# Optimization experiments

Measured on AMD Instinct MI355X. Metric: run time of the kernel, lower is better.

## Reference

```python
import jax, jax.numpy as jnp
import numpy as np

N, E, DIN, H, C = 50000, 800000, 256, 128, 8


def setup_inputs() -> dict:
    key = jax.random.key(0)
    k1, k2, k3, k4 = jax.random.split(key, 4)
    x = jax.random.normal(k1, (N, DIN), dtype=jnp.float32)
    edge_index = jax.random.randint(k2, (2, E), 0, N, dtype=jnp.int64)
    W1 = jax.random.normal(k3, (DIN, H), dtype=jnp.float32) * (1.0 / np.sqrt(DIN))
    b1 = jnp.zeros((H,), dtype=jnp.float32)
    W2 = jax.random.normal(k4, (H, C), dtype=jnp.float32) * (1.0 / np.sqrt(H))
    b2 = jnp.zeros((C,), dtype=jnp.float32)
    return {"x": x, "W1": W1, "b1": b1, "W2": W2, "b2": b2, "edge_index": edge_index}


def reference(x, W1, b1, W2, b2, edge_index):
    n = x.shape[0]
    loop = jnp.arange(n, dtype=edge_index.dtype)
    src = jnp.concatenate([edge_index[0], loop])  # messages flow src -> dst
    dst = jnp.concatenate([edge_index[1], loop])
    # symmetric GCN normalization with self-loops (PyG GCNConv default)
    deg = jax.ops.segment_sum(jnp.ones_like(dst, dtype=x.dtype), dst, num_segments=n)
    dinv = jnp.where(deg > 0, deg ** -0.5, 0.0)
    norm = dinv[src] * dinv[dst]  # [E+N]

    def gcn_layer(h, W, b):
        h = h @ W                                   # [N, d_out]
        msg = norm[:, None] * h[src]                # gather: [E+N, d_out]
        agg = jax.ops.segment_sum(msg, dst, num_segments=n)  # scatter-add
        return agg + b

    h = jax.nn.relu(gcn_layer(x, W1, b1))
    # F.dropout(training=False) is identity in eval mode
    out = gcn_layer(h, W2, b2)
    return jax.nn.log_softmax(out, axis=1)
```

## Files before the change

kernel.cpp:

```cpp
#include <hip/hip_runtime.h>
#include <hip/hip_bf16.h>
#include <hip/hip_fp16.h>
#include <stdint.h>

#define DIN 256
#define HD  128
#define CD  8
#define KCH 64
#define SBW 72
#define CSRW 64
#define ECH 4096
#define CAP 64

typedef __attribute__((ext_vector_type(8))) short bf16x8;
typedef __attribute__((ext_vector_type(4))) float f32x4;

__device__ __forceinline__ float bf2f(unsigned short u) {
    union { unsigned int i; float f; } v; v.i = ((unsigned int)u) << 16; return v.f;
}
__device__ __forceinline__ unsigned short f2bf(float f) {
    union { float f; unsigned int i; } v; v.f = f;
    unsigned int r = v.i + 0x7fffu + ((v.i >> 16) & 1u);
    return (unsigned short)(r >> 16);
}
__device__ __forceinline__ int edge_at(const void* ei, int is64, long long idx) {
    return is64 ? (int)((const long long*)ei)[idx] : ((const int*)ei)[idx];
}

__global__ __launch_bounds__(256) void prep_kernel(
    const float* __restrict__ W1, unsigned short* __restrict__ W1T)
{
    int tg = blockIdx.x * 256 + threadIdx.x;
    if (tg < HD * (DIN / 4)) {
        int n  = tg & (HD - 1);
        int k4 = (tg >> 7) * 4;
        unsigned short v[4];
#pragma unroll
        for (int j = 0; j < 4; j++) v[j] = f2bf(W1[(k4 + j) * HD + n]);
        *reinterpret_cast<unsigned long long*>(W1T + (size_t)n * DIN + k4) =
            ((unsigned long long)v[0]) | ((unsigned long long)v[1] << 16) |
            ((unsigned long long)v[2] << 32) | ((unsigned long long)v[3] << 48);
    }
}

__global__ __launch_bounds__(256) void gemm1_scatter_kernel(
    const float* __restrict__ x, const unsigned short* __restrict__ W1T,
    unsigned short* __restrict__ h, int M,
    const void* __restrict__ ei,
    unsigned int* __restrict__ ebuf, unsigned int* __restrict__ G,
    int E, int N, int G1, int NB)
{
    __shared__ unsigned short w1t[HD * SBW];
    if ((int)blockIdx.x >= G1) {
        int* cur = (int*)w1t;
        const int tid = threadIdx.x;
        cur[tid] = 0;
        __syncthreads();
        const int lane = tid & 63;
        int oddw = ((const int*)ei)[2 * lane + 1];
        unsigned long long zb = __ballot(oddw == 0);
        int is64 = (__popcll(zb) >= 56) ? 1 : 0;
        const int c = (int)blockIdx.x - G1;
        const long long e0 = (long long)c * ECH;
#pragma unroll
        for (int k = 0; k < ECH / 256; k++) {
            long long e = e0 + tid + k * 256;
            if (e < E) {
                int s = edge_at(ei, is64, e);
                int d = edge_at(ei, is64, (long long)E + e);
                if ((unsigned)d < (unsigned)N && (unsigned)s < (unsigned)N) {
                    int b = ((unsigned)d) >> 8;
                    int p = atomicAdd(&cur[b], 1);
                    if (p < CAP)
                        ebuf[((size_t)b * NB + c) * CAP + p] =
                            (unsigned int)s | ((unsigned int)d << 16);
                }
            }
        }
        __syncthreads();
        int v = cur[tid]; if (v > CAP) v = CAP;
        G[(size_t)c * 256 + tid] = (unsigned int)v;
        return;
    }
    const int tid  = threadIdx.x;
    const int lane = tid & 63;
    const int wave = tid >> 6;
    const int quad = lane >> 4;
    const int r15  = lane & 15;
    const long long rowBase = (long long)blockIdx.x * 128 + wave * 32;

    f32x4 acc[2][8];
#pragma unroll
    for (int rt = 0; rt < 2; rt++)
#pragma unroll
        for (int ct = 0; ct < 8; ct++)
#pragma unroll
            for (int i = 0; i < 4; i++) acc[rt][ct][i] = 0.0f;

    for (int kh = 0; kh < DIN / KCH; kh++) {
        __syncthreads();
        for (int c = tid; c < HD * (KCH / 8); c += 256) {
            int n   = c >> 3;
            int kk0 = (c & 7) * 8;
            bf16x8 v = *reinterpret_cast<const bf16x8*>(W1T + (size_t)n * DIN + kh * KCH + kk0);
            *reinterpret_cast<bf16x8*>(&w1t[n * SBW + kk0]) = v;
        }
        __syncthreads();

        for (int ki = 0; ki < KCH / 32; ki++) {
            int kk0 = ki * 32 + quad * 8;
            int kg  = kh * KCH + kk0;
            bf16x8 a[2];
#pragma unroll
            for (int rt = 0; rt < 2; rt++) {
                long long row = rowBase + rt * 16 + r15;
                if (row < M) {
                    const float* xp = x + row * DIN + kg;
                    f32x4 f0 = *reinterpret_cast<const f32x4*>(xp);
                    f32x4 f1 = *reinterpret_cast<const f32x4*>(xp + 4);
#pragma unroll
                    for (int j = 0; j < 4; j++) {
                        a[rt][j]     = (short)f2bf(f0[j]);
                        a[rt][j + 4] = (short)f2bf(f1[j]);
                    }
                } else {
#pragma unroll
                    for (int j = 0; j < 8; j++) a[rt][j] = 0;
                }
            }
#pragma unroll
            for (int ct = 0; ct < 8; ct++) {
                bf16x8 b = *reinterpret_cast<const bf16x8*>(&w1t[(ct * 16 + r15) * SBW + kk0]);
                acc[0][ct] = __builtin_amdgcn_mfma_f32_16x16x32_bf16(a[0], b, acc[0][ct], 0, 0, 0);
                acc[1][ct] = __builtin_amdgcn_mfma_f32_16x16x32_bf16(a[1], b, acc[1][ct], 0, 0, 0);
            }
        }
    }
#pragma unroll
    for (int rt = 0; rt < 2; rt++)
#pragma unroll
        for (int ct = 0; ct < 8; ct++)
#pragma unroll
            for (int i = 0; i < 4; i++) {
                long long row = rowBase + rt * 16 + quad * 4 + i;
                if (row < M) h[row * HD + ct * 16 + r15] = f2bf(acc[rt][ct][i]);
            }
}

__global__ __launch_bounds__(256) void csr_build_kernel(
    const unsigned int* __restrict__ ebuf, const unsigned int* __restrict__ G,
    unsigned short* __restrict__ colf, int* __restrict__ count, int N, int NB)
{
    __shared__ int cnt[256];
    __shared__ int gcnt[256];
    const int b = blockIdx.x;
    const int tid = threadIdx.x;
    cnt[tid] = 0;
    gcnt[tid] = (tid < NB) ? (int)G[(size_t)tid * 256 + b] : 0;
    __syncthreads();
    const size_t basee = (size_t)b * NB * CAP;
    const int tot = NB * CAP;
    for (int idx = tid; idx < tot; idx += 256) {
        int c = idx >> 6;
        int i = idx & (CAP - 1);
        if (i < gcnt[c]) {
            unsigned int e = ebuf[basee + idx];
            int d = (int)(e >> 16);
            int slot = atomicAdd(&cnt[d & 255], 1);
            if (slot < CSRW) colf[(d << 6) + slot] = (unsigned short)(e & 0xFFFFu);
        }
    }
    __syncthreads();
    int n = (b << 8) + tid;
    if (n < N) count[n] = cnt[tid];
}

__global__ __launch_bounds__(256) void scale_kernel(
    const unsigned short* __restrict__ h, const int* __restrict__ count,
    unsigned short* __restrict__ h2, int N)
{
    int t = blockIdx.x * 256 + threadIdx.x;
    if (t >= N * (HD / 8)) return;
    int n = t >> 4;
    int deg = count[n]; if (deg > CSRW) deg = CSRW;
    float dn = rsqrtf((float)deg + 1.0f);
    bf16x8 v = *reinterpret_cast<const bf16x8*>(h + (size_t)t * 8);
    bf16x8 o;
#pragma unroll
    for (int j = 0; j < 8; j++) {
        float f = bf2f((unsigned short)v[j]) * dn;
        __half hf = __float2half(f);
        o[j] = *reinterpret_cast<short*>(&hf);
    }
    *reinterpret_cast<bf16x8*>(h2 + (size_t)t * 8) = o;
}

__global__ __launch_bounds__(256) void agg1_fused_kernel(
    const unsigned short* __restrict__ h2, const int* __restrict__ count,
    const unsigned short* __restrict__ colf, const float* __restrict__ b1,
    const float* __restrict__ W2, float* __restrict__ hw2, int N)
{
    const int lane = threadIdx.x & 63;
    const int n = blockIdx.x * 4 + (threadIdx.x >> 6);
    if (n >= N) return;

    float w2a[CD], w2b[CD];
#pragma unroll
    for (int c = 0; c < CD; c++) {
        w2a[c] = W2[(2 * lane)     * CD + c];
        w2b[c] = W2[(2 * lane + 1) * CD + c];
    }

    int deg = count[n]; if (deg > CSRW) deg = CSRW;
    const float dn = rsqrtf((float)deg + 1.0f);

    union UH { unsigned int u; __half2 h; };
    UH p; p.u = *reinterpret_cast<const unsigned int*>(h2 + ((size_t)n << 7) + 2 * lane);
    float2 pf = __half22float2(p.h);
    float acc0 = pf.x, acc1 = pf.y;

    const int base = n << 6;
    int i = 0;
    for (; i + 7 < deg; i += 8) {
        unsigned long long c0 = *reinterpret_cast<const unsigned long long*>(colf + base + i);
        unsigned long long c1 = *reinterpret_cast<const unsigned long long*>(colf + base + i + 4);
        unsigned int s[8];
#pragma unroll
        for (int j = 0; j < 4; j++) {
            s[j]     = (unsigned int)((c0 >> (16 * j)) & 0xFFFFu);
            s[j + 4] = (unsigned int)((c1 >> (16 * j)) & 0xFFFFu);
        }
        UH hv[8];
#pragma unroll
        for (int j = 0; j < 8; j++)
            hv[j].u = *reinterpret_cast<const unsigned int*>(h2 + ((size_t)s[j] << 7) + 2 * lane);
#pragma unroll
        for (int j = 0; j < 8; j++) {
            float2 f = __half22float2(hv[j].h);
            acc0 += f.x;
            acc1 += f.y;
        }
    }
    for (; i < deg; i++) {
        unsigned int s0 = colf[base + i];
        UH a; a.u = *reinterpret_cast<const unsigned int*>(h2 + ((size_t)s0 << 7) + 2 * lane);
        float2 f = __half22float2(a.h);
        acc0 += f.x;
        acc1 += f.y;
    }

    float v0 = dn * acc0 + b1[2 * lane];     v0 = v0 > 0.0f ? v0 : 0.0f;
    float v1 = dn * acc1 + b1[2 * lane + 1]; v1 = v1 > 0.0f ? v1 : 0.0f;

    float part[CD];
#pragma unroll
    for (int c = 0; c < CD; c++) part[c] = v0 * w2a[c] + v1 * w2b[c];

    float t4[4];
    {
        int hi = lane & 1;
#pragma unroll
        for (int k = 0; k < 4; k++) {
            float send = hi ? part[k] : part[4 + k];
            float recv = __shfl_xor(send, 1, 64);
            t4[k] = (hi ? part[4 + k] : part[k]) + recv;
        }
    }
    float t2[2];
    {
        int hi = (lane >> 1) & 1;
#pragma unroll
        for (int k = 0; k < 2; k++) {
            float send = hi ? t4[k] : t4[2 + k];
            float recv = __shfl_xor(send, 2, 64);
            t2[k] = (hi ? t4[2 + k] : t4[k]) + recv;
        }
    }
    float t1;
    {
        int hi = (lane >> 2) & 1;
        float send = hi ? t2[0] : t2[1];
        float recv = __shfl_xor(send, 4, 64);
        t1 = (hi ? t2[1] : t2[0]) + recv;
    }
    t1 += __shfl_xor(t1, 8, 64);
    t1 += __shfl_xor(t1, 16, 64);
    t1 += __shfl_xor(t1, 32, 64);
    int c = ((lane & 1) << 2) | (lane & 2) | ((lane >> 2) & 1);
    if (lane < CD) hw2[(size_t)n * CD + c] = dn * t1;
}

__global__ __launch_bounds__(256) void agg2_kernel(
    const float* __restrict__ hw2, const int* __restrict__ count,
    const unsigned short* __restrict__ colf, const float* __restrict__ b2,
    float* __restrict__ out, int N) {
    int n = blockIdx.x * 256 + threadIdx.x;
    if (n >= N) return;
    int deg = count[n]; if (deg > CSRW) deg = CSRW;
    float dn = rsqrtf((float)deg + 1.0f);
    f32x4 a0 = *reinterpret_cast<const f32x4*>(hw2 + (size_t)n * CD);
    f32x4 a1 = *reinterpret_cast<const f32x4*>(hw2 + (size_t)n * CD + 4);
    const int base = n << 6;
    int i = 0;
    for (; i + 3 < deg; i += 4) {
        unsigned long long cc = *reinterpret_cast<const unsigned long long*>(colf + base + i);
        unsigned int s0 = (unsigned int)(cc & 0xFFFFu);
        unsigned int s1 = (unsigned int)((cc >> 16) & 0xFFFFu);
        unsigned int s2 = (unsigned int)((cc >> 32) & 0xFFFFu);
        unsigned int s3 = (unsigned int)((cc >> 48) & 0xFFFFu);
        f32x4 b0 = *reinterpret_cast<const f32x4*>(hw2 + (size_t)s0 * CD);
        f32x4 b1v = *reinterpret_cast<const f32x4*>(hw2 + (size_t)s0 * CD + 4);
        f32x4 c0 = *reinterpret_cast<const f32x4*>(hw2 + (size_t)s1 * CD);
        f32x4 c1 = *reinterpret_cast<const f32x4*>(hw2 + (size_t)s1 * CD + 4);
        f32x4 d0 = *reinterpret_cast<const f32x4*>(hw2 + (size_t)s2 * CD);
        f32x4 d1 = *reinterpret_cast<const f32x4*>(hw2 + (size_t)s2 * CD + 4);
        f32x4 e0 = *reinterpret_cast<const f32x4*>(hw2 + (size_t)s3 * CD);
        f32x4 e1 = *reinterpret_cast<const f32x4*>(hw2 + (size_t)s3 * CD + 4);
        a0 += (b0 + c0) + (d0 + e0);
        a1 += (b1v + c1) + (d1 + e1);
    }
    for (; i < deg; i++) {
        unsigned int s0 = colf[base + i];
        a0 += *reinterpret_cast<const f32x4*>(hw2 + (size_t)s0 * CD);
        a1 += *reinterpret_cast<const f32x4*>(hw2 + (size_t)s0 * CD + 4);
    }
    float v[CD];
#pragma unroll
    for (int j = 0; j < 4; j++) {
        v[j]     = dn * a0[j] + b2[j];
        v[4 + j] = dn * a1[j] + b2[4 + j];
    }
    float mx = v[0];
#pragma unroll
    for (int j = 1; j < CD; j++) mx = fmaxf(mx, v[j]);
    float s8 = 0.0f;
#pragma unroll
    for (int j = 0; j < CD; j++) s8 += expf(v[j] - mx);
    float lse = mx + logf(s8);
    f32x4 o0, o1;
#pragma unroll
    for (int j = 0; j < 4; j++) {
        o0[j] = v[j] - lse;
        o1[j] = v[4 + j] - lse;
    }
    *reinterpret_cast<f32x4*>(out + (size_t)n * CD)     = o0;
    *reinterpret_cast<f32x4*>(out + (size_t)n * CD + 4) = o1;
}

extern "C" void kernel_launch(void* const* d_in, const int* in_sizes, int n_in,
                              void* d_out, int out_size, void* d_ws, size_t ws_size,
                              hipStream_t stream) {
    const float* x  = (const float*)d_in[0];
    const float* W1 = (const float*)d_in[1];
    const float* b1 = (const float*)d_in[2];
    const float* W2 = (const float*)d_in[3];
    const float* b2 = (const float*)d_in[4];
    const void*  ei = d_in[5];
    const int N = in_sizes[0] / DIN;
    const int E = in_sizes[5] / 2;
    const int G1 = (N + 127) / 128;
    const int NB = (E + ECH - 1) / ECH;
    const int NBK = (N + 255) / 256;

    char* ws = (char*)d_ws;
    size_t off = 0;
    auto alloc = [&](size_t bytes) -> void* {
        void* p = ws + off;
        off = (off + bytes + 255) & ~(size_t)255;
        return p;
    };
    int*   count = (int*)alloc((size_t)N * 4);
    unsigned short* colf = (unsigned short*)alloc((size_t)N * CSRW * 2);
    unsigned short* h  = (unsigned short*)alloc((size_t)N * HD * 2);
    unsigned short* h2 = (unsigned short*)alloc((size_t)N * HD * 2);
    float* hw2 = (float*)alloc((size_t)N * CD * 4);
    unsigned short* W1T = (unsigned short*)alloc((size_t)HD * DIN * 2);
    unsigned int* G    = (unsigned int*)alloc((size_t)NB * 256 * 4);
    unsigned int* ebuf = (unsigned int*)alloc((size_t)NB * 256 * CAP * 4);

    prep_kernel         <<<32, 256, 0, stream>>>(W1, W1T);
    gemm1_scatter_kernel<<<G1 + NB, 256, 0, stream>>>(x, W1T, h, N, ei, ebuf, G, E, N, G1, NB);
    csr_build_kernel    <<<NBK, 256, 0, stream>>>(ebuf, G, colf, count, N, NB);
    scale_kernel        <<<(N * (HD / 8) + 255) / 256, 256, 0, stream>>>(h, count, h2, N);
    agg1_fused_kernel   <<<(N + 3) / 4, 256, 0, stream>>>(h2, count, colf, b1, W2, hw2, N);
    agg2_kernel         <<<(N + 255) / 256, 256, 0, stream>>>(hw2, count, colf, b2,
                                                              (float*)d_out, N);
}
```

Baseline: 196.0 us.

## Fuse degree scaling into CSR build and preload full neighbor list in aggregation

```diff
diff --git a/kernel.cpp b/kernel.cpp
--- a/kernel.cpp
+++ b/kernel.cpp
@@ -14,6 +14,7 @@
 
 typedef __attribute__((ext_vector_type(8))) short bf16x8;
 typedef __attribute__((ext_vector_type(4))) float f32x4;
+typedef __attribute__((ext_vector_type(4))) unsigned int u32x4;
 
 __device__ __forceinline__ float bf2f(unsigned short u) {
     union { unsigned int i; float f; } v; v.i = ((unsigned int)u) << 16; return v.f;
@@ -149,6 +150,7 @@
 
 __global__ __launch_bounds__(256) void csr_build_kernel(
     const unsigned int* __restrict__ ebuf, const unsigned int* __restrict__ G,
+    const unsigned short* __restrict__ h, unsigned short* __restrict__ h2,
     unsigned short* __restrict__ colf, int* __restrict__ count, int N, int NB)
 {
     __shared__ int cnt[256];
@@ -173,26 +175,23 @@
     __syncthreads();
     int n = (b << 8) + tid;
     if (n < N) count[n] = cnt[tid];
-}
-
-__global__ __launch_bounds__(256) void scale_kernel(
-    const unsigned short* __restrict__ h, const int* __restrict__ count,
-    unsigned short* __restrict__ h2, int N)
-{
-    int t = blockIdx.x * 256 + threadIdx.x;
-    if (t >= N * (HD / 8)) return;
-    int n = t >> 4;
-    int deg = count[n]; if (deg > CSRW) deg = CSRW;
-    float dn = rsqrtf((float)deg + 1.0f);
-    bf16x8 v = *reinterpret_cast<const bf16x8*>(h + (size_t)t * 8);
-    bf16x8 o;
-#pragma unroll
-    for (int j = 0; j < 8; j++) {
-        float f = bf2f((unsigned short)v[j]) * dn;
-        __half hf = __float2half(f);
-        o[j] = *reinterpret_cast<short*>(&hf);
-    }
-    *reinterpret_cast<bf16x8*>(h2 + (size_t)t * 8) = o;
+    for (int t = tid; t < 256 * 16; t += 256) {
+        int ln = t >> 4;
+        int gn = (b << 8) + ln;
+        if (gn < N) {
+            int dg = cnt[ln]; if (dg > CSRW) dg = CSRW;
+            float dnn = rsqrtf((float)dg + 1.0f);
+            bf16x8 v = *reinterpret_cast<const bf16x8*>(h + ((size_t)gn << 7) + (t & 15) * 8);
+            bf16x8 o;
+#pragma unroll
+            for (int j = 0; j < 8; j++) {
+                float f = bf2f((unsigned short)v[j]) * dnn;
+                __half hf = __float2half(f);
+                o[j] = *reinterpret_cast<short*>(&hf);
+            }
+            *reinterpret_cast<bf16x8*>(h2 + ((size_t)gn << 7) + (t & 15) * 8) = o;
+        }
+    }
 }
 
 __global__ __launch_bounds__(256) void agg1_fused_kernel(
@@ -204,54 +203,52 @@
     const int n = blockIdx.x * 4 + (threadIdx.x >> 6);
     if (n >= N) return;
 
-    float w2a[CD], w2b[CD];
-#pragma unroll
-    for (int c = 0; c < CD; c++) {
-        w2a[c] = W2[(2 * lane)     * CD + c];
-        w2b[c] = W2[(2 * lane + 1) * CD + c];
-    }
-
     int deg = count[n]; if (deg > CSRW) deg = CSRW;
     const float dn = rsqrtf((float)deg + 1.0f);
+
+    const u32x4* cfq = reinterpret_cast<const u32x4*>(colf + ((size_t)n << 6));
+    u32x4 q0 = cfq[0], q1 = cfq[1], q2 = cfq[2], q3 = cfq[3],
+          q4 = cfq[4], q5 = cfq[5], q6 = cfq[6], q7 = cfq[7];
 
     union UH { unsigned int u; __half2 h; };
     UH p; p.u = *reinterpret_cast<const unsigned int*>(h2 + ((size_t)n << 7) + 2 * lane);
     float2 pf = __half22float2(p.h);
     float acc0 = pf.x, acc1 = pf.y;
 
-    const int base = n << 6;
-    int i = 0;
-    for (; i + 7 < deg; i += 8) {
-        unsigned long long c0 = *reinterpret_cast<const unsigned long long*>(colf + base + i);
-        unsigned long long c1 = *reinterpret_cast<const unsigned long long*>(colf + base + i + 4);
-        unsigned int s[8];
-#pragma unroll
-        for (int j = 0; j < 4; j++) {
-            s[j]     = (unsigned int)((c0 >> (16 * j)) & 0xFFFFu);
-            s[j + 4] = (unsigned int)((c1 >> (16 * j)) & 0xFFFFu);
-        }
-        UH hv[8];
-#pragma unroll
-        for (int j = 0; j < 8; j++)
-            hv[j].u = *reinterpret_cast<const unsigned int*>(h2 + ((size_t)s[j] << 7) + 2 * lane);
-#pragma unroll
-        for (int j = 0; j < 8; j++) {
-            float2 f = __half22float2(hv[j].h);
-            acc0 += f.x;
-            acc1 += f.y;
-        }
-    }
-    for (; i < deg; i++) {
-        unsigned int s0 = colf[base + i];
-        UH a; a.u = *reinterpret_cast<const unsigned int*>(h2 + ((size_t)s0 << 7) + 2 * lane);
-        float2 f = __half22float2(a.h);
-        acc0 += f.x;
-        acc1 += f.y;
-    }
+#define AGG_GRP(q, gb)                                                         \
+    if (deg > (gb)) {                                                          \
+        unsigned int s_[8];                                                    \
+        s_[0] = q[0] & 0xFFFFu;  s_[1] = q[0] >> 16;                           \
+        s_[2] = q[1] & 0xFFFFu;  s_[3] = q[1] >> 16;                           \
+        s_[4] = q[2] & 0xFFFFu;  s_[5] = q[2] >> 16;                           \
+        s_[6] = q[3] & 0xFFFFu;  s_[7] = q[3] >> 16;                           \
+        UH hv_[8];                                                             \
+        _Pragma("unroll")                                                      \
+        for (int j = 0; j < 8; j++) {                                          \
+            hv_[j].u = ((gb) + j < deg)                                        \
+                ? *reinterpret_cast<const unsigned int*>(                      \
+                      h2 + ((size_t)s_[j] << 7) + 2 * lane)                    \
+                : 0u;                                                          \
+        }                                                                      \
+        _Pragma("unroll")                                                      \
+        for (int j = 0; j < 8; j++) {                                          \
+            float2 f_ = __half22float2(hv_[j].h);                              \
+            acc0 += f_.x; acc1 += f_.y;                                        \
+        }                                                                      \
+    }
+    AGG_GRP(q0, 0)  AGG_GRP(q1, 8)  AGG_GRP(q2, 16) AGG_GRP(q3, 24)
+    AGG_GRP(q4, 32) AGG_GRP(q5, 40) AGG_GRP(q6, 48) AGG_GRP(q7, 56)
+#undef AGG_GRP
 
     float v0 = dn * acc0 + b1[2 * lane];     v0 = v0 > 0.0f ? v0 : 0.0f;
     float v1 = dn * acc1 + b1[2 * lane + 1]; v1 = v1 > 0.0f ? v1 : 0.0f;
 
+    float w2a[CD], w2b[CD];
+#pragma unroll
+    for (int c = 0; c < CD; c++) {
+        w2a[c] = W2[(2 * lane)     * CD + c];
+        w2b[c] = W2[(2 * lane + 1) * CD + c];
+    }
     float part[CD];
 #pragma unroll
     for (int c = 0; c < CD; c++) part[c] = v0 * w2a[c] + v1 * w2b[c];
@@ -380,8 +377,7 @@
 
     prep_kernel         <<<32, 256, 0, stream>>>(W1, W1T);
     gemm1_scatter_kernel<<<G1 + NB, 256, 0, stream>>>(x, W1T, h, N, ei, ebuf, G, E, N, G1, NB);
-    csr_build_kernel    <<<NBK, 256, 0, stream>>>(ebuf, G, colf, count, N, NB);
-    scale_kernel        <<<(N * (HD / 8) + 255) / 256, 256, 0, stream>>>(h, count, h2, N);
+    csr_build_kernel    <<<NBK, 256, 0, stream>>>(ebuf, G, h, h2, colf, count, N, NB);
     agg1_fused_kernel   <<<(N + 3) / 4, 256, 0, stream>>>(h2, count, colf, b1, W2, hw2, N);
     agg2_kernel         <<<(N + 255) / 256, 256, 0, stream>>>(hw2, count, colf, b2,
                                                               (float*)d_out, N);
```

Measured after the change: 190.5 us. 1.03x faster.
